# Performance work log

Measured on AMD Instinct MI355X. Metric: run time of the kernel, lower is better.

Reference implementation:

```python
import jax, jax.numpy as jnp
import numpy as np
import math

B, N, DIM = 4, 2048, 768
HEADS, DIM_HEAD = 12, 64
SCALE = math.sqrt(DIM_HEAD)


def setup_inputs() -> dict:
    key = jax.random.key(0)
    ks = jax.random.split(key, 5)
    inner = HEADS * DIM_HEAD
    x = jax.random.normal(ks[0], (B, N, DIM), dtype=jnp.float32)
    # Linear weights stored as [in, out] so y = x @ W (equivalent to torch Linear with W.T)
    w_q = jax.random.normal(ks[1], (DIM, inner), dtype=jnp.float32) * 0.02
    w_k = jax.random.normal(ks[2], (DIM, inner), dtype=jnp.float32) * 0.02
    w_v = jax.random.normal(ks[3], (DIM, inner), dtype=jnp.float32) * 0.02
    w_o = jax.random.normal(ks[4], (inner, DIM), dtype=jnp.float32) * 0.02
    b_o = jnp.zeros((DIM,), dtype=jnp.float32)
    return {"x": x, "w_q": w_q, "w_k": w_k, "w_v": w_v, "w_o": w_o, "b_o": b_o}


def _split_heads(t):
    # [b, n, h*d] -> [b, h, n, d]
    b, n, _ = t.shape
    return t.reshape(b, n, HEADS, DIM_HEAD).transpose(0, 2, 1, 3)


def reference(x, w_q, w_k, w_v, w_o, b_o):
    # context = x (self-attention, kv_include_self=False)
    q = _split_heads(x @ w_q)  # [b,h,n,d]
    k = _split_heads(x @ w_k)
    v = _split_heads(x @ w_v)
    scores = jnp.einsum("bhnd,bhmd->bhnm", q, k) / SCALE  # [b,h,n,n]
    attn = jax.nn.softmax(scores, axis=-1)  # dropout p=0 -> identity
    h = jnp.einsum("bhnm,bhmd->bhnd", attn, v)  # [b,h,n,d]
    H = h.transpose(0, 2, 1, 3).reshape(x.shape[0], x.shape[1], HEADS * DIM_HEAD)
    out = H @ w_o + b_o
    return out
```

## Files before the change

### kernel.cpp

```cpp
#include <hip/hip_runtime.h>
#include <hip/hip_bf16.h>
#include <cstdint>
#include <cstddef>

#define HEADS 12
#define DHEAD 64
#define SEQ   2048
#define DIMM  768
#define BATCH 4
#define MROWS (BATCH*SEQ)
#define BH    (BATCH*HEADS)
#define SCL_Q 0.18033688011112042f

typedef __attribute__((ext_vector_type(8))) short short8;
typedef __attribute__((ext_vector_type(4))) short short4v;
typedef __attribute__((ext_vector_type(4))) float floatx4;

__device__ __forceinline__ unsigned short f2bf(float f) {
    union { float f; uint32_t u; } v; v.f = f;
    uint32_t u = v.u;
    u += 0x7fffu + ((u >> 16) & 1u);
    return (unsigned short)(u >> 16);
}
__device__ __forceinline__ float bf2f(unsigned short h) {
    union { uint32_t u; float f; } v; v.u = ((uint32_t)h) << 16;
    return v.f;
}
#if __has_builtin(__builtin_amdgcn_perm)
__device__ __forceinline__ uint32_t pkbf(float a, float b) {
    union { float f; uint32_t u; } ua, ub; ua.f = a; ub.f = b;
    return __builtin_amdgcn_perm(ub.u + 0x8000u, ua.u + 0x8000u, 0x07060302u);
}
#else
__device__ __forceinline__ uint32_t pkbf(float a, float b) {
    __hip_bfloat162 h = __float22bfloat162_rn(make_float2(a, b));
    uint32_t u; __builtin_memcpy(&u, &h, 4); return u;
}
#endif
__device__ __forceinline__ float fexp2(float x) {
#if __has_builtin(__builtin_amdgcn_exp2f)
    return __builtin_amdgcn_exp2f(x);
#else
    return exp2f(x);
#endif
}

#if __has_builtin(__builtin_amdgcn_global_load_lds)
#define HAVE_GLDS 1
__device__ __forceinline__ void glds16(const unsigned short* g, unsigned short* l) {
    __builtin_amdgcn_global_load_lds(
        (const __attribute__((address_space(1))) unsigned int*)g,
        (__attribute__((address_space(3))) unsigned int*)l, 16, 0, 0);
}
#else
#define HAVE_GLDS 0
#endif

__device__ __forceinline__ int detect_f32(const uint32_t* xw, int tid) {
    __shared__ int cnt_;
    if (tid == 0) cnt_ = 0;
    __syncthreads();
    uint32_t w = xw[(size_t)(tid & 255) * 4096];
    float av = fabsf(bf2f((unsigned short)(w & 0xFFFFu)));
    atomicAdd(&cnt_, (av >= 9.0949e-13f && av <= 256.0f) ? 1 : 0);
    __syncthreads();
    return (cnt_ < 192) ? 1 : 0;
}

__global__ __launch_bounds__(256) void prep(
    const void* __restrict__ x,
    const void* __restrict__ wq, const void* __restrict__ wk,
    const void* __restrict__ wv, const void* __restrict__ wo,
    unsigned short* __restrict__ xc,
    unsigned short* __restrict__ wtq, unsigned short* __restrict__ wtk,
    unsigned short* __restrict__ wtv, unsigned short* __restrict__ wto)
{
    const int tid = threadIdx.x;
    const int isf32 = detect_f32((const uint32_t*)x, tid);
    const int blk = blockIdx.x;

    if (blk < 2304) {
        __shared__ unsigned short tile[32][33];
        const int m = blk / 576, rr = blk % 576;
        const void* src; unsigned short* dst;
        switch (m) {
            case 0: src = wq; dst = wtq; break;
            case 1: src = wk; dst = wtk; break;
            case 2: src = wv; dst = wtv; break;
            default: src = wo; dst = wto; break;
        }
        const float* srcf = (const float*)src;
        const unsigned short* srcs = (const unsigned short*)src;
        const int tx = tid & 31, ty = tid >> 5;
        const int k0 = (rr % 24) * 32;
        const int n0 = (rr / 24) * 32;
        #pragma unroll
        for (int it = 0; it < 4; it++) {
            int r = ty + it * 8;
            size_t idx = (size_t)(k0 + r) * DIMM + n0 + tx;
            tile[r][tx] = isf32 ? f2bf(srcf[idx]) : srcs[idx];
        }
        __syncthreads();
        #pragma unroll
        for (int it = 0; it < 4; it++) {
            int r = ty + it * 8;
            dst[(size_t)(n0 + r) * DIMM + k0 + tx] = tile[tx][r];
        }
    } else {
        const size_t i0 = ((size_t)(blk - 2304) * 256 + tid) * 8;
        if (isf32) {
            const float* xf = (const float*)x;
            float4 a = *(const float4*)&xf[i0];
            float4 b = *(const float4*)&xf[i0 + 4];
            short8 s = { (short)f2bf(a.x), (short)f2bf(a.y), (short)f2bf(a.z), (short)f2bf(a.w),
                         (short)f2bf(b.x), (short)f2bf(b.y), (short)f2bf(b.z), (short)f2bf(b.w) };
            *(short8*)&xc[i0] = s;
        } else {
            *(short8*)&xc[i0] = *(const short8*)&((const unsigned short*)x)[i0];
        }
    }
}

__global__ __launch_bounds__(256) void gemm_bt(
    const unsigned short* __restrict__ A,
    const unsigned short* __restrict__ Wt0,
    const unsigned short* __restrict__ Wt1,
    const unsigned short* __restrict__ Wt2,
    void* __restrict__ O0, void* __restrict__ O1, void* __restrict__ O2,
    const void* __restrict__ bias,
    const uint32_t* __restrict__ xsample,
    int mode_base)
{
    const int mode = mode_base + blockIdx.z;
    const unsigned short* Wt = (mode == 1) ? Wt1 : (mode == 2) ? Wt2 : Wt0;
    void* OutV               = (mode == 1) ? O1  : (mode == 2) ? O2  : O0;
    unsigned short* Out16 = (unsigned short*)OutV;
    float* Outf           = (float*)OutV;

    int isf32 = 0;
    if (mode == 3) isf32 = detect_f32(xsample, threadIdx.x);

    __shared__ unsigned short As[128 * 64];
    __shared__ unsigned short Bs[128 * 64];

    const int tid  = threadIdx.x;
    const int wid  = tid >> 6;
    const int lane = tid & 63;
    const int l16  = lane & 15;
    const int quad = lane >> 4;
    const int wm   = wid & 1;
    const int wn   = wid >> 1;
    const int bm   = blockIdx.x * 128;
    const int bn   = blockIdx.y * 128;
    const bool swap = (mode != 2);

    floatx4 acc[4][4];
    #pragma unroll
    for (int i = 0; i < 4; i++)
        #pragma unroll
        for (int j = 0; j < 4; j++)
            acc[i][j] = floatx4{0.f, 0.f, 0.f, 0.f};

    for (int kk = 0; kk < DIMM; kk += 64) {
        #pragma unroll
        for (int t = 0; t < 4; t++) {
            const int c  = t * 256 + tid;
            const int r  = c >> 3;
            const int lc = (((c & 7) ^ (r & 7))) * 8;
#if HAVE_GLDS
            glds16(&A [(size_t)(bm + r) * DIMM + kk + lc], &As[(t * 256 + wid * 64) * 8]);
            glds16(&Wt[(size_t)(bn + r) * DIMM + kk + lc], &Bs[(t * 256 + wid * 64) * 8]);
#else
            *(short8*)&As[c * 8] = *(const short8*)&A [(size_t)(bm + r) * DIMM + kk + lc];
            *(short8*)&Bs[c * 8] = *(const short8*)&Wt[(size_t)(bn + r) * DIMM + kk + lc];
#endif
        }
        __syncthreads();
        #pragma unroll
        for (int ks = 0; ks < 2; ks++) {
            const int ph = ((ks * 4 + quad) ^ (l16 & 7)) * 8;
            short8 xa[4], wb[4];
            #pragma unroll
            for (int t = 0; t < 4; t++)
                xa[t] = *(const short8*)&As[(wm * 64 + t * 16 + l16) * 64 + ph];
            #pragma unroll
            for (int t = 0; t < 4; t++)
                wb[t] = *(const short8*)&Bs[(wn * 64 + t * 16 + l16) * 64 + ph];
            if (swap) {
                #pragma unroll
                for (int mt = 0; mt < 4; mt++)
                    #pragma unroll
                    for (int nt = 0; nt < 4; nt++)
                        acc[mt][nt] = __builtin_amdgcn_mfma_f32_16x16x32_bf16(
                            wb[mt], xa[nt], acc[mt][nt], 0, 0, 0);
            } else {
                #pragma unroll
                for (int mt = 0; mt < 4; mt++)
                    #pragma unroll
                    for (int nt = 0; nt < 4; nt++)
                        acc[mt][nt] = __builtin_amdgcn_mfma_f32_16x16x32_bf16(
                            xa[mt], wb[nt], acc[mt][nt], 0, 0, 0);
            }
        }
        __syncthreads();
    }

    if (!swap) {
        #pragma unroll
        for (int nt = 0; nt < 4; nt++) {
            const int gcol = bn + wn * 64 + nt * 16 + l16;
            #pragma unroll
            for (int mt = 0; mt < 4; mt++) {
                const int grow0 = bm + wm * 64 + mt * 16 + quad * 4;
                const int b = grow0 >> 11, n0 = grow0 & 2047;
                const int h = gcol >> 6,  d  = gcol & 63;
                size_t addr = ((size_t)(b * HEADS + h) * DHEAD + d) * SEQ + n0;
                short4v pk = { (short)f2bf(acc[mt][nt][0]), (short)f2bf(acc[mt][nt][1]),
                               (short)f2bf(acc[mt][nt][2]), (short)f2bf(acc[mt][nt][3]) };
                *(short4v*)&Out16[addr] = pk;
            }
        }
    } else {
        #pragma unroll
        for (int nt = 0; nt < 4; nt++) {
            const int grow = bm + wm * 64 + nt * 16 + l16;
            #pragma unroll
            for (int mt = 0; mt < 4; mt++) {
                const int gcol0 = bn + wn * 64 + mt * 16 + quad * 4;
                float v0 = acc[mt][nt][0], v1 = acc[mt][nt][1];
                float v2 = acc[mt][nt][2], v3 = acc[mt][nt][3];
                if (mode == 0) { v0 *= SCL_Q; v1 *= SCL_Q; v2 *= SCL_Q; v3 *= SCL_Q; }
                if (mode == 3) {
                    if (isf32) {
                        float4 bv = *(const float4*)&((const float*)bias)[gcol0];
                        float4 o = { v0 + bv.x, v1 + bv.y, v2 + bv.z, v3 + bv.w };
                        *(float4*)&Outf[(size_t)grow * DIMM + gcol0] = o;
                    } else {
                        const unsigned short* bb = &((const unsigned short*)bias)[gcol0];
                        short4v pk = { (short)f2bf(v0 + bf2f(bb[0])),
                                       (short)f2bf(v1 + bf2f(bb[1])),
                                       (short)f2bf(v2 + bf2f(bb[2])),
                                       (short)f2bf(v3 + bf2f(bb[3])) };
                        *(short4v*)&Out16[(size_t)grow * DIMM + gcol0] = pk;
                    }
                } else {
                    const int b = grow >> 11, n = grow & 2047;
                    const int h = gcol0 >> 6, d = gcol0 & 63;
                    size_t addr = ((size_t)(b * HEADS + h) * SEQ + n) * DHEAD + d;
                    short4v pk = { (short)f2bf(v0), (short)f2bf(v1),
                                   (short)f2bf(v2), (short)f2bf(v3) };
                    *(short4v*)&Out16[addr] = pk;
                }
            }
        }
    }
}

__global__ __launch_bounds__(256) void gemm_o64(
    const unsigned short* __restrict__ A,
    const unsigned short* __restrict__ Wt,
    void* __restrict__ Out,
    const void* __restrict__ bias,
    const uint32_t* __restrict__ xsample)
{
    unsigned short* Out16 = (unsigned short*)Out;
    float* Outf           = (float*)Out;
    const int isf32 = detect_f32(xsample, threadIdx.x);

    __shared__ unsigned short As[128 * 64];
    __shared__ unsigned short Bs[64 * 64];

    const int tid  = threadIdx.x;
    const int wid  = tid >> 6;
    const int lane = tid & 63;
    const int l16  = lane & 15;
    const int quad = lane >> 4;
    const int wm   = wid & 1;
    const int wn   = wid >> 1;
    const int bm   = blockIdx.x * 128;
    const int bn   = blockIdx.y * 64;

    floatx4 acc[2][4];
    #pragma unroll
    for (int i = 0; i < 2; i++)
        #pragma unroll
        for (int j = 0; j < 4; j++)
            acc[i][j] = floatx4{0.f, 0.f, 0.f, 0.f};

    for (int kk = 0; kk < DIMM; kk += 64) {
        #pragma unroll
        for (int t = 0; t < 4; t++) {
            const int c  = t * 256 + tid;
            const int r  = c >> 3;
            const int lc = (((c & 7) ^ (r & 7))) * 8;
#if HAVE_GLDS
            glds16(&A[(size_t)(bm + r) * DIMM + kk + lc], &As[(t * 256 + wid * 64) * 8]);
#else
            *(short8*)&As[c * 8] = *(const short8*)&A[(size_t)(bm + r) * DIMM + kk + lc];
#endif
        }
        #pragma unroll
        for (int t = 0; t < 2; t++) {
            const int c  = t * 256 + tid;
            const int r  = c >> 3;
            const int lc = (((c & 7) ^ (r & 7))) * 8;
#if HAVE_GLDS
            glds16(&Wt[(size_t)(bn + r) * DIMM + kk + lc], &Bs[(t * 256 + wid * 64) * 8]);
#else
            *(short8*)&Bs[c * 8] = *(const short8*)&Wt[(size_t)(bn + r) * DIMM + kk + lc];
#endif
        }
        __syncthreads();
        #pragma unroll
        for (int ks = 0; ks < 2; ks++) {
            const int ph = ((ks * 4 + quad) ^ (l16 & 7)) * 8;
            short8 xa[4], wb[2];
            #pragma unroll
            for (int t = 0; t < 4; t++)
                xa[t] = *(const short8*)&As[(wm * 64 + t * 16 + l16) * 64 + ph];
            #pragma unroll
            for (int t = 0; t < 2; t++)
                wb[t] = *(const short8*)&Bs[(wn * 32 + t * 16 + l16) * 64 + ph];
            #pragma unroll
            for (int mt = 0; mt < 2; mt++)
                #pragma unroll
                for (int nt = 0; nt < 4; nt++)
                    acc[mt][nt] = __builtin_amdgcn_mfma_f32_16x16x32_bf16(
                        wb[mt], xa[nt], acc[mt][nt], 0, 0, 0);
        }
        __syncthreads();
    }

    #pragma unroll
    for (int nt = 0; nt < 4; nt++) {
        const int grow = bm + wm * 64 + nt * 16 + l16;
        #pragma unroll
        for (int mt = 0; mt < 2; mt++) {
            const int gcol0 = bn + wn * 32 + mt * 16 + quad * 4;
            const float v0 = acc[mt][nt][0], v1 = acc[mt][nt][1];
            const float v2 = acc[mt][nt][2], v3 = acc[mt][nt][3];
            if (isf32) {
                float4 bv = *(const float4*)&((const float*)bias)[gcol0];
                float4 o = { v0 + bv.x, v1 + bv.y, v2 + bv.z, v3 + bv.w };
                *(float4*)&Outf[(size_t)grow * DIMM + gcol0] = o;
            } else {
                const unsigned short* bb = &((const unsigned short*)bias)[gcol0];
                short4v pk = { (short)f2bf(v0 + bf2f(bb[0])),
                               (short)f2bf(v1 + bf2f(bb[1])),
                               (short)f2bf(v2 + bf2f(bb[2])),
                               (short)f2bf(v3 + bf2f(bb[3])) };
                *(short4v*)&Out16[(size_t)grow * DIMM + gcol0] = pk;
            }
        }
    }
}

__global__ __launch_bounds__(256, 3) void attn(
    const unsigned short* __restrict__ Q,
    const unsigned short* __restrict__ K,
    const unsigned short* __restrict__ Vt,
    unsigned short* __restrict__ Hout)
{
    __shared__ unsigned short Ks[64 * 72];
    __shared__ unsigned short Vs[64 * 72];
    __shared__ unsigned short Ps[8][16 * 72];

    const int tid  = threadIdx.x;
    const int wid  = tid >> 6;
    const int lane = tid & 63;
    const int l16  = lane & 15;
    const int quad = lane >> 4;

    const int bh = blockIdx.x % BH;
    const int qt = blockIdx.x / BH;

    short8 qf[2][2];
    #pragma unroll
    for (int t = 0; t < 2; t++) {
        const int qrow = qt * 128 + wid * 32 + t * 16 + l16;
        const size_t qbase = ((size_t)bh * SEQ + qrow) * DHEAD;
        qf[t][0] = *(const short8*)&Q[qbase + quad * 8];
        qf[t][1] = *(const short8*)&Q[qbase + 32 + quad * 8];
    }

    const short8 ones = { (short)0x3F80, (short)0x3F80, (short)0x3F80, (short)0x3F80,
                          (short)0x3F80, (short)0x3F80, (short)0x3F80, (short)0x3F80 };

    floatx4 ot[2][4];
    floatx4 acc_l[2];
    #pragma unroll
    for (int t = 0; t < 2; t++) {
        acc_l[t] = floatx4{0.f, 0.f, 0.f, 0.f};
        #pragma unroll
        for (int i = 0; i < 4; i++) ot[t][i] = floatx4{0.f, 0.f, 0.f, 0.f};
    }

    const size_t kbase = (size_t)bh * SEQ * DHEAD;
    const size_t vbase = (size_t)bh * DHEAD * SEQ;

    short8 rk[2], rv[2];
    #pragma unroll
    for (int j = 0; j < 2; j++) {
        const int c = tid + j * 256, r = c >> 3, c8 = (c & 7) * 8;
        rk[j] = *(const short8*)&K[kbase + (size_t)r * DHEAD + c8];
        rv[j] = *(const short8*)&Vt[vbase + (size_t)r * SEQ + c8];
    }

    short8 vfr[2][4];
    short8 pfr[2][2];

    for (int kt = 0; kt < SEQ / 64; kt++) {
        if (kt > 0) {
            #pragma unroll
            for (int ks = 0; ks < 2; ks++) {
                #pragma unroll
                for (int dt = 0; dt < 4; dt++)
                    vfr[ks][dt] = *(const short8*)&Vs[(dt * 16 + l16) * 72 + ks * 32 + quad * 8];
                #pragma unroll
                for (int t = 0; t < 2; t++)
                    pfr[ks][t] = *(const short8*)&Ps[wid * 2 + t][l16 * 72 + ks * 32 + quad * 8];
            }
        }
        __syncthreads();
        #pragma unroll
        for (int j = 0; j < 2; j++) {
            const int c = tid + j * 256, r = c >> 3, c8 = (c & 7) * 8;
            *(short8*)&Ks[r * 72 + c8] = rk[j];
            *(short8*)&Vs[r * 72 + c8] = rv[j];
        }
        __syncthreads();
        if (kt + 1 < SEQ / 64) {
            #pragma unroll
            for (int j = 0; j < 2; j++) {
                const int c = tid + j * 256, r = c >> 3, c8 = (c & 7) * 8;
                rk[j] = *(const short8*)&K[kbase + (size_t)((kt + 1) * 64 + r) * DHEAD + c8];
                rv[j] = *(const short8*)&Vt[vbase + (size_t)r * SEQ + (kt + 1) * 64 + c8];
            }
        }

        uint2 pk[2][4];
        #pragma unroll
        for (int mt = 0; mt < 4; mt++) {
            short8 kf0 = *(const short8*)&Ks[(mt * 16 + l16) * 72 + quad * 8];
            short8 kf1 = *(const short8*)&Ks[(mt * 16 + l16) * 72 + 32 + quad * 8];
            #pragma unroll
            for (int t = 0; t < 2; t++) {
                floatx4 a = floatx4{0.f, 0.f, 0.f, 0.f};
                a = __builtin_amdgcn_mfma_f32_16x16x32_bf16(kf0, qf[t][0], a, 0, 0, 0);
                a = __builtin_amdgcn_mfma_f32_16x16x32_bf16(kf1, qf[t][1], a, 0, 0, 0);
                pk[t][mt] = (uint2){ pkbf(fexp2(a[0]), fexp2(a[1])),
                                     pkbf(fexp2(a[2]), fexp2(a[3])) };
            }
        }

        if (kt > 0) {
            __builtin_amdgcn_s_setprio(1);
            #pragma unroll
            for (int ks = 0; ks < 2; ks++) {
                #pragma unroll
                for (int t = 0; t < 2; t++) {
                    #pragma unroll
                    for (int dt = 0; dt < 4; dt++)
                        ot[t][dt] = __builtin_amdgcn_mfma_f32_16x16x32_bf16(
                            vfr[ks][dt], pfr[ks][t], ot[t][dt], 0, 0, 0);
                    acc_l[t] = __builtin_amdgcn_mfma_f32_16x16x32_bf16(
                        ones, pfr[ks][t], acc_l[t], 0, 0, 0);
                }
            }
            __builtin_amdgcn_s_setprio(0);
        }

        #pragma unroll
        for (int t = 0; t < 2; t++)
            #pragma unroll
            for (int mt = 0; mt < 4; mt++)
                *(uint2*)&Ps[wid * 2 + t][l16 * 72 + mt * 16 + quad * 4] = pk[t][mt];
    }

    {
        #pragma unroll
        for (int ks = 0; ks < 2; ks++) {
            #pragma unroll
            for (int dt = 0; dt < 4; dt++)
                vfr[ks][dt] = *(const short8*)&Vs[(dt * 16 + l16) * 72 + ks * 32 + quad * 8];
            #pragma unroll
            for (int t = 0; t < 2; t++)
                pfr[ks][t] = *(const short8*)&Ps[wid * 2 + t][l16 * 72 + ks * 32 + quad * 8];
        }
        __builtin_amdgcn_s_setprio(1);
        #pragma unroll
        for (int ks = 0; ks < 2; ks++)
            #pragma unroll
            for (int t = 0; t < 2; t++) {
                #pragma unroll
                for (int dt = 0; dt < 4; dt++)
                    ot[t][dt] = __builtin_amdgcn_mfma_f32_16x16x32_bf16(
                        vfr[ks][dt], pfr[ks][t], ot[t][dt], 0, 0, 0);
                acc_l[t] = __builtin_amdgcn_mfma_f32_16x16x32_bf16(
                    ones, pfr[ks][t], acc_l[t], 0, 0, 0);
            }
        __builtin_amdgcn_s_setprio(0);
    }

    const int b = bh / HEADS, h = bh % HEADS;
    #pragma unroll
    for (int t = 0; t < 2; t++) {
        const float inv_l = 1.0f / acc_l[t][0];
        unsigned short* Pw = Ps[wid * 2 + t];
        #pragma unroll
        for (int dt = 0; dt < 4; dt++) {
            uint2 pk2 = { pkbf(ot[t][dt][0] * inv_l, ot[t][dt][1] * inv_l),
                          pkbf(ot[t][dt][2] * inv_l, ot[t][dt][3] * inv_l) };
            *(uint2*)&Pw[l16 * 72 + dt * 16 + quad * 4] = pk2;
        }
        const int q_r   = lane >> 2;
        const int dpart = (lane & 3) * 16;
        short8 h0 = *(const short8*)&Pw[q_r * 72 + dpart];
        short8 h1 = *(const short8*)&Pw[q_r * 72 + dpart + 8];
        const int growg = b * SEQ + qt * 128 + wid * 32 + t * 16 + q_r;
        const size_t oaddr = (size_t)growg * DIMM + h * DHEAD + dpart;
        *(short8*)&Hout[oaddr] = h0;
        *(short8*)&Hout[oaddr + 8] = h1;
    }
}

extern "C" void kernel_launch(void* const* d_in, const int* in_sizes, int n_in,
                              void* d_out, int out_size, void* d_ws, size_t ws_size,
                              hipStream_t stream)
{
    (void)in_sizes; (void)n_in; (void)out_size;
    const void* x  = d_in[0];
    const void* wq = d_in[1];
    const void* wk = d_in[2];
    const void* wv = d_in[3];
    const void* wo = d_in[4];
    const void* bo = d_in[5];

    char* ws = (char*)d_ws;
    const size_t SZ_QKV = (size_t)MROWS * DIMM * sizeof(unsigned short);
    const size_t SZ_W   = (size_t)DIMM * DIMM * sizeof(unsigned short);
    const size_t need = 5 * SZ_QKV + 4 * SZ_W;
    if (ws_size < need) return;

    unsigned short* xc   = (unsigned short*)(ws);
    unsigned short* Qws  = (unsigned short*)(ws + 1 * SZ_QKV);
    unsigned short* Kws  = (unsigned short*)(ws + 2 * SZ_QKV);
    unsigned short* Vtws = (unsigned short*)(ws + 3 * SZ_QKV);
    unsigned short* Hws  = (unsigned short*)(ws + 4 * SZ_QKV);
    unsigned short* Wtq  = (unsigned short*)(ws + 5 * SZ_QKV);
    unsigned short* Wtk  = (unsigned short*)(ws + 5 * SZ_QKV + SZ_W);
    unsigned short* Wtv  = (unsigned short*)(ws + 5 * SZ_QKV + 2 * SZ_W);
    unsigned short* Wto  = (unsigned short*)(ws + 5 * SZ_QKV + 3 * SZ_W);

    hipLaunchKernelGGL(prep, dim3(2304 + MROWS * DIMM / 2048), dim3(256), 0, stream,
                       x, wq, wk, wv, wo, xc, Wtq, Wtk, Wtv, Wto);
    hipLaunchKernelGGL(gemm_bt, dim3(64, 6, 3), dim3(256), 0, stream,
                       xc, Wtq, Wtk, Wtv, (void*)Qws, (void*)Kws, (void*)Vtws,
                       bo, (const uint32_t*)x, 0);
    hipLaunchKernelGGL(attn, dim3(BH * (SEQ / 128)), dim3(256), 0, stream,
                       Qws, Kws, Vtws, Hws);
    hipLaunchKernelGGL(gemm_o64, dim3(64, 12), dim3(256), 0, stream,
                       Hws, Wto, d_out, bo, (const uint32_t*)x);
}
```

Baseline: 238.5 us.

## Double-buffer K/V tiles in LDS with XOR swizzle, dropping one barrier

The attention kernel now keeps two LDS buffers for the K and V tiles and prefetches global data two tiles ahead. This lets it remove one of the two __syncthreads per KV iteration. LDS rows shrink from 72 to 64 elements and use an XOR swizzle on 8-element chunks instead of padding to avoid bank conflicts. LDS footprint grows, which may affect occupancy at 3 blocks per CU, and the swizzle adds index arithmetic.

```diff
diff --git a/kernel.cpp b/kernel.cpp
--- a/kernel.cpp
+++ b/kernel.cpp
@@ -361,15 +361,16 @@
     const unsigned short* __restrict__ Vt,
     unsigned short* __restrict__ Hout)
 {
-    __shared__ unsigned short Ks[64 * 72];
-    __shared__ unsigned short Vs[64 * 72];
-    __shared__ unsigned short Ps[8][16 * 72];
+    __shared__ unsigned short KsB[2 * 64 * 64];
+    __shared__ unsigned short VsB[2 * 64 * 64];
+    __shared__ unsigned short Ps[8][16 * 64];
 
     const int tid  = threadIdx.x;
     const int wid  = tid >> 6;
     const int lane = tid & 63;
     const int l16  = lane & 15;
     const int quad = lane >> 4;
+    const int sw   = l16 & 7;
 
     const int bh = blockIdx.x % BH;
     const int qt = blockIdx.x / BH;
@@ -402,47 +403,63 @@
     #pragma unroll
     for (int j = 0; j < 2; j++) {
         const int c = tid + j * 256, r = c >> 3, c8 = (c & 7) * 8;
-        rk[j] = *(const short8*)&K[kbase + (size_t)r * DHEAD + c8];
-        rv[j] = *(const short8*)&Vt[vbase + (size_t)r * SEQ + c8];
+        const int g = ((c & 7) ^ (r & 7)) * 8;
+        short8 tk = *(const short8*)&K[kbase + (size_t)r * DHEAD + c8];
+        short8 tv = *(const short8*)&Vt[vbase + (size_t)r * SEQ + c8];
+        *(short8*)&KsB[r * 64 + g] = tk;
+        *(short8*)&VsB[r * 64 + g] = tv;
+        rk[j] = *(const short8*)&K[kbase + (size_t)(64 + r) * DHEAD + c8];
+        rv[j] = *(const short8*)&Vt[vbase + (size_t)r * SEQ + 64 + c8];
     }
 
     short8 vfr[2][4];
     short8 pfr[2][2];
 
     for (int kt = 0; kt < SEQ / 64; kt++) {
+        const int cur = kt & 1;
+        unsigned short* Kc = &KsB[cur * 4096];
+        unsigned short* Kn = &KsB[(cur ^ 1) * 4096];
+        unsigned short* Vn = &VsB[(cur ^ 1) * 4096];
+
         if (kt > 0) {
             #pragma unroll
             for (int ks = 0; ks < 2; ks++) {
                 #pragma unroll
                 for (int dt = 0; dt < 4; dt++)
-                    vfr[ks][dt] = *(const short8*)&Vs[(dt * 16 + l16) * 72 + ks * 32 + quad * 8];
+                    vfr[ks][dt] = *(const short8*)
+                        &Vn[(dt * 16 + l16) * 64 + ((ks * 4 + quad) ^ sw) * 8];
                 #pragma unroll
                 for (int t = 0; t < 2; t++)
-                    pfr[ks][t] = *(const short8*)&Ps[wid * 2 + t][l16 * 72 + ks * 32 + quad * 8];
+                    pfr[ks][t] = *(const short8*)
+                        &Ps[wid * 2 + t][l16 * 64 + ((ks * 4 + quad) ^ sw) * 8];
             }
         }
         __syncthreads();
-        #pragma unroll
-        for (int j = 0; j < 2; j++) {
-            const int c = tid + j * 256, r = c >> 3, c8 = (c & 7) * 8;
-            *(short8*)&Ks[r * 72 + c8] = rk[j];
-            *(short8*)&Vs[r * 72 + c8] = rv[j];
-        }
-        __syncthreads();
+
         if (kt + 1 < SEQ / 64) {
+            #pragma unroll
+            for (int j = 0; j < 2; j++) {
+                const int c = tid + j * 256, r = c >> 3;
+                const int g = ((c & 7) ^ (r & 7)) * 8;
+                *(short8*)&Kn[r * 64 + g] = rk[j];
+                *(short8*)&Vn[r * 64 + g] = rv[j];
+            }
+        }
+        if (kt + 2 < SEQ / 64) {
             #pragma unroll
             for (int j = 0; j < 2; j++) {
                 const int c = tid + j * 256, r = c >> 3, c8 = (c & 7) * 8;
-                rk[j] = *(const short8*)&K[kbase + (size_t)((kt + 1) * 64 + r) * DHEAD + c8];
-                rv[j] = *(const short8*)&Vt[vbase + (size_t)r * SEQ + (kt + 1) * 64 + c8];
+                rk[j] = *(const short8*)&K[kbase + (size_t)((kt + 2) * 64 + r) * DHEAD + c8];
+                rv[j] = *(const short8*)&Vt[vbase + (size_t)r * SEQ + (kt + 2) * 64 + c8];
             }
         }
 
         uint2 pk[2][4];
         #pragma unroll
         for (int mt = 0; mt < 4; mt++) {
-            short8 kf0 = *(const short8*)&Ks[(mt * 16 + l16) * 72 + quad * 8];
-            short8 kf1 = *(const short8*)&Ks[(mt * 16 + l16) * 72 + 32 + quad * 8];
+            const int krow = (mt * 16 + l16) * 64;
+            short8 kf0 = *(const short8*)&Kc[krow + (quad ^ sw) * 8];
+            short8 kf1 = *(const short8*)&Kc[krow + ((4 + quad) ^ sw) * 8];
             #pragma unroll
             for (int t = 0; t < 2; t++) {
                 floatx4 a = floatx4{0.f, 0.f, 0.f, 0.f};
@@ -474,18 +491,23 @@
         for (int t = 0; t < 2; t++)
             #pragma unroll
             for (int mt = 0; mt < 4; mt++)
-                *(uint2*)&Ps[wid * 2 + t][l16 * 72 + mt * 16 + quad * 4] = pk[t][mt];
+                *(uint2*)&Ps[wid * 2 + t]
+                    [l16 * 64 + ((2 * mt + (quad >> 1)) ^ sw) * 8 + (quad & 1) * 4]
+                    = pk[t][mt];
     }
 
     {
+        unsigned short* Vl = &VsB[((SEQ / 64 - 1) & 1) * 4096];
         #pragma unroll
         for (int ks = 0; ks < 2; ks++) {
             #pragma unroll
             for (int dt = 0; dt < 4; dt++)
-                vfr[ks][dt] = *(const short8*)&Vs[(dt * 16 + l16) * 72 + ks * 32 + quad * 8];
+                vfr[ks][dt] = *(const short8*)
+                    &Vl[(dt * 16 + l16) * 64 + ((ks * 4 + quad) ^ sw) * 8];
             #pragma unroll
             for (int t = 0; t < 2; t++)
-                pfr[ks][t] = *(const short8*)&Ps[wid * 2 + t][l16 * 72 + ks * 32 + quad * 8];
+                pfr[ks][t] = *(const short8*)
+                    &Ps[wid * 2 + t][l16 * 64 + ((ks * 4 + quad) ^ sw) * 8];
         }
         __builtin_amdgcn_s_setprio(1);
         #pragma unroll
@@ -511,12 +533,14 @@
         for (int dt = 0; dt < 4; dt++) {
             uint2 pk2 = { pkbf(ot[t][dt][0] * inv_l, ot[t][dt][1] * inv_l),
                           pkbf(ot[t][dt][2] * inv_l, ot[t][dt][3] * inv_l) };
-            *(uint2*)&Pw[l16 * 72 + dt * 16 + quad * 4] = pk2;
+            *(uint2*)&Pw[l16 * 64 + ((2 * dt + (quad >> 1)) ^ sw) * 8 + (quad & 1) * 4]
+                = pk2;
         }
         const int q_r   = lane >> 2;
         const int dpart = (lane & 3) * 16;
-        short8 h0 = *(const short8*)&Pw[q_r * 72 + dpart];
-        short8 h1 = *(const short8*)&Pw[q_r * 72 + dpart + 8];
+        const int rsw   = q_r & 7;
+        short8 h0 = *(const short8*)&Pw[q_r * 64 + ((2 * (lane & 3)) ^ rsw) * 8];
+        short8 h1 = *(const short8*)&Pw[q_r * 64 + ((2 * (lane & 3) + 1) ^ rsw) * 8];
         const int growg = b * SEQ + qt * 128 + wid * 32 + t * 16 + q_r;
         const size_t oaddr = (size_t)growg * DIMM + h * DHEAD + dpart;
         *(short8*)&Hout[oaddr] = h0;
```

New measurement: 233.5 us. 1.02x faster.
